# Optimization experiments

Hardware: AMD Instinct MI355X
Metric: run time of the kernel (lower is better)

The kernel has to match this reference:

```python
import jax, jax.numpy as jnp
import numpy as np
import math

H = 1024
N = 64  # state size; N2 = N // 2 complex modes
DT_MIN, DT_MAX = 0.001, 0.1


def setup_inputs() -> dict:
    key = jax.random.key(0)
    k1, k2 = jax.random.split(key)
    N2 = N // 2
    # C is declared zeros in the buggy source; use randn so the output is non-trivial
    C = jax.random.normal(k1, (H, N2), dtype=jnp.float32)
    log_dt = math.log(DT_MIN) + jax.random.uniform(k2, (H,), dtype=jnp.float32) * (
        math.log(DT_MAX) - math.log(DT_MIN)
    )
    log_A_real = jnp.full((H, N2), math.log(0.5), dtype=jnp.float32)
    A_imag = math.pi * jnp.broadcast_to(jnp.arange(N2, dtype=jnp.float32), (H, N2))
    return {
        "C": C,
        "log_dt": log_dt,
        "log_A_real": log_A_real,
        "A_imag": A_imag,
        "L": 4096,
    }


def reference(C, log_dt, log_A_real, A_imag, L):
    dt = jnp.exp(log_dt)  # (H,)
    A = -jnp.exp(log_A_real) + 1j * A_imag  # (H, N2) complex
    dtA = A * dt[:, None].astype(A.dtype)  # (H, N2)
    # Vandermonde: exp(dtA[h,n] * l) for l in [0, L)  -> (H, N2, L)
    P = jnp.exp(dtA[:, :, None] * jnp.arange(L, dtype=jnp.float32))
    Cc = C.astype(dtA.dtype) * (jnp.exp(dtA) - 1.0) / A  # (H, N2)
    K = 2.0 * jnp.einsum("hn,hnl->hl", Cc, P)  # (H, L) complex
    return K.real
```

## Files before the change

kernel.cpp:

```cpp
#include <hip/hip_runtime.h>


static __device__ __forceinline__ float bcast0(float x) {
    return __uint_as_float(__builtin_amdgcn_readfirstlane(__float_as_uint(x)));
}

static __device__ __forceinline__ float2 cmul(float2 a, float2 b) {
    return make_float2(fmaf(a.x, b.x, -(a.y * b.y)),
                       fmaf(a.x, b.y,   a.y * b.x));
}

template <int N2, int BLK, int J>
__global__ __launch_bounds__(BLK, 4) void s4d_kernel(
    const float* __restrict__ C,
    const float* __restrict__ log_dt,
    const float* __restrict__ log_A_real,
    const float* __restrict__ A_imag,
    float* __restrict__ K,
    int L, int lbase)
{
    __shared__ float2 s_lo[N2][16];
    __shared__ float2 s_hi[N2][16];
    __shared__ float2 s_W[N2];

    const int h = blockIdx.x;
    const int t = threadIdx.x;

    if (t < N2) {
        const int n = t;
        const float dt  = expf(log_dt[h]);
        const float Are = -expf(log_A_real[h * N2 + n]);
        const float Aim = A_imag[h * N2 + n];
        const float dre = Are * dt;
        const float dim = Aim * dt;
        float sw, cw;
        sincosf(dim, &sw, &cw);
        const float er = expf(dre);
        const float2 w = make_float2(er * cw, er * sw);
        const float nre = w.x - 1.0f;
        const float nim = w.y;
        const float inv = 1.0f / (Are * Are + Aim * Aim);
        const float qre = (nre * Are + nim * Aim) * inv;
        const float qim = (nim * Are - nre * Aim) * inv;
        const float c2  = 2.0f * C[h * N2 + n];
        float2 cur = make_float2(c2 * qre, c2 * qim);
#pragma unroll
        for (int k = 0; k < 16; ++k) { s_lo[n][k] = cur; cur = cmul(cur, w); }
        const float2 w2  = cmul(w,  w);
        const float2 w4  = cmul(w2, w2);
        const float2 w8  = cmul(w4, w4);
        const float2 w16 = cmul(w8, w8);
        float2 curh = make_float2(1.0f, 0.0f);
#pragma unroll
        for (int k = 0; k < 16; ++k) { s_hi[n][k] = curh; curh = cmul(curh, w16); }
        s_W[n] = curh;
    }
    __syncthreads();

    float acc[J];
#pragma unroll
    for (int j = 0; j < J; ++j) acc[j] = 0.0f;

    const int tlo = t & 15;
    const int thi = t >> 4;

#pragma unroll 4
    for (int n = 0; n < N2; ++n) {
        const float2 lo = s_lo[n][tlo];
        const float2 hi = s_hi[n][thi];
        const float Wre = bcast0(s_W[n].x);
        const float Wim = bcast0(s_W[n].y);

        float sre = fmaf(lo.x, hi.x, -(lo.y * hi.y));
        float smi = fmaf(lo.x, hi.y,   lo.y * hi.x);

#pragma unroll
        for (int j = 0; j < J - 1; ++j) {
            acc[j] += sre;
            const float tr = fmaf(sre, Wre, -(smi * Wim));
            smi = fmaf(sre, Wim, smi * Wre);
            sre = tr;
        }
        acc[J - 1] += sre;
    }

    float* __restrict__ outp = K + (size_t)h * (size_t)L + lbase + t;
#pragma unroll
    for (int j = 0; j < J; ++j) {
        const int l = lbase + j * BLK + t;
        if (l < L) outp[(size_t)j * BLK] = acc[j];
    }
}

extern "C" void kernel_launch(void* const* d_in, const int* in_sizes, int n_in,
                              void* d_out, int out_size, void* d_ws, size_t ws_size,
                              hipStream_t stream)
{
    const float* C          = (const float*)d_in[0];
    const float* log_dt     = (const float*)d_in[1];
    const float* log_A_real = (const float*)d_in[2];
    const float* A_imag     = (const float*)d_in[3];
    float* K = (float*)d_out;

    const int H  = in_sizes[1];
    const int N2 = in_sizes[0] / H;
    const int L  = out_size / H;
    constexpr int BLK = 256;
    constexpr int J   = 16;

    if (N2 != 32) return;
    for (int lbase = 0; lbase < L; lbase += BLK * J) {
        s4d_kernel<32, BLK, J><<<H, BLK, 0, stream>>>(
            C, log_dt, log_A_real, A_imag, K, L, lbase);
    }
}
```

Measured before the change: 84.49 us.

## Use real second-order recurrence and 2D grid instead of complex stepping

Replaces the complex rotation per output step with a real two-term linear recurrence x_{j+2}=2Re(W)x_{j+1}-|W|^2 x_j, seeded by two precomputed starting terms stored in a second shared table. This cuts the multiply-adds per step from about four to two. The L range is now split over a second grid dimension with a smaller J, and the per-block starting offset is computed by exponentiation by squaring, so one launch replaces the host loop. Occupancy hint is raised to 8. The recurrence may accumulate error differently, especially where |W| is close to 1.

```diff
diff --git a/kernel.cpp b/kernel.cpp
--- a/kernel.cpp
+++ b/kernel.cpp
@@ -11,19 +11,22 @@
 }
 
 template <int N2, int BLK, int J>
-__global__ __launch_bounds__(BLK, 4) void s4d_kernel(
+__global__ __launch_bounds__(BLK, 8) void s4d_kernel(
     const float* __restrict__ C,
     const float* __restrict__ log_dt,
     const float* __restrict__ log_A_real,
     const float* __restrict__ A_imag,
     float* __restrict__ K,
-    int L, int lbase)
+    int L)
 {
-    __shared__ float2 s_lo[N2][16];
-    __shared__ float2 s_hi[N2][16];
-    __shared__ float2 s_W[N2];
+    __shared__ float2 s_lo [N2][16];
+    __shared__ float2 s_lo2[N2][16];
+    __shared__ float2 s_hi [N2][16];
+    __shared__ float2 s_ab [N2];
 
     const int h = blockIdx.x;
+    const int y = blockIdx.y;
+    const int lbase = y * (BLK * J);
     const int t = threadIdx.x;
 
     if (t < N2) {
@@ -43,9 +46,6 @@
         const float qre = (nre * Are + nim * Aim) * inv;
         const float qim = (nim * Are - nre * Aim) * inv;
         const float c2  = 2.0f * C[h * N2 + n];
-        float2 cur = make_float2(c2 * qre, c2 * qim);
-#pragma unroll
-        for (int k = 0; k < 16; ++k) { s_lo[n][k] = cur; cur = cmul(cur, w); }
         const float2 w2  = cmul(w,  w);
         const float2 w4  = cmul(w2, w2);
         const float2 w8  = cmul(w4, w4);
@@ -53,7 +53,19 @@
         float2 curh = make_float2(1.0f, 0.0f);
 #pragma unroll
         for (int k = 0; k < 16; ++k) { s_hi[n][k] = curh; curh = cmul(curh, w16); }
-        s_W[n] = curh;
+        const float2 W = curh;
+        s_ab[n] = make_float2(W.x + W.x, -fmaf(W.x, W.x, W.y * W.y));
+        float2 P = make_float2(1.0f, 0.0f);
+        float2 base = W;
+        int e = J * y;
+        while (e) { if (e & 1) P = cmul(P, base); base = cmul(base, base); e >>= 1; }
+        float2 cur  = cmul(make_float2(c2 * qre, c2 * qim), P);
+        float2 cur2 = cmul(cur, W);
+#pragma unroll
+        for (int k = 0; k < 16; ++k) {
+            s_lo [n][k] = cur;  cur  = cmul(cur,  w);
+            s_lo2[n][k] = cur2; cur2 = cmul(cur2, w);
+        }
     }
     __syncthreads();
 
@@ -64,24 +76,25 @@
     const int tlo = t & 15;
     const int thi = t >> 4;
 
-#pragma unroll 4
+#pragma unroll 2
     for (int n = 0; n < N2; ++n) {
-        const float2 lo = s_lo[n][tlo];
-        const float2 hi = s_hi[n][thi];
-        const float Wre = bcast0(s_W[n].x);
-        const float Wim = bcast0(s_W[n].y);
+        const float2 lo  = s_lo [n][tlo];
+        const float2 lo2 = s_lo2[n][tlo];
+        const float2 hi  = s_hi [n][thi];
+        const float  aW  = bcast0(s_ab[n].x);
+        const float  bW  = bcast0(s_ab[n].y);
 
-        float sre = fmaf(lo.x, hi.x, -(lo.y * hi.y));
-        float smi = fmaf(lo.x, hi.y,   lo.y * hi.x);
-
+        float x0 = fmaf(lo.x,  hi.x, -(lo.y  * hi.y));
+        float x1 = fmaf(lo2.x, hi.x, -(lo2.y * hi.y));
+        acc[0] += x0;
+        acc[1] += x1;
 #pragma unroll
-        for (int j = 0; j < J - 1; ++j) {
-            acc[j] += sre;
-            const float tr = fmaf(sre, Wre, -(smi * Wim));
-            smi = fmaf(sre, Wim, smi * Wre);
-            sre = tr;
+        for (int j = 2; j < J; ++j) {
+            const float x2 = fmaf(aW, x1, bW * x0);
+            acc[j] += x2;
+            x0 = x1;
+            x1 = x2;
         }
-        acc[J - 1] += sre;
     }
 
     float* __restrict__ outp = K + (size_t)h * (size_t)L + lbase + t;
@@ -102,15 +115,15 @@
     const float* A_imag     = (const float*)d_in[3];
     float* K = (float*)d_out;
 
-    const int H  = in_sizes[1];
-    const int N2 = in_sizes[0] / H;
-    const int L  = out_size / H;
+    const int H   = in_sizes[1];
+    const int N2v = in_sizes[0] / H;
+    const int L   = out_size / H;
     constexpr int BLK = 256;
-    constexpr int J   = 16;
+    constexpr int J   = 8;
+    const int gy = (L + BLK * J - 1) / (BLK * J);
 
-    if (N2 != 32) return;
-    for (int lbase = 0; lbase < L; lbase += BLK * J) {
-        s4d_kernel<32, BLK, J><<<H, BLK, 0, stream>>>(
-            C, log_dt, log_A_real, A_imag, K, L, lbase);
-    }
+    if (N2v != 32) return;
+    dim3 grid((unsigned)H, (unsigned)gy);
+    s4d_kernel<32, BLK, J><<<grid, BLK, 0, stream>>>(
+        C, log_dt, log_A_real, A_imag, K, L);
 }
```

New measurement: 81.12 us. 1.04x faster.
